# Kernel optimization log

Hardware: AMD Instinct MI355X
Metric: run time of the kernel (lower is better)

The kernel has to match this reference:

```python
import jax, jax.numpy as jnp
import numpy as np

ALPHA = 0.2  # LeakyReLU negative slope
MASK_VAL = -1e9


def setup_inputs() -> dict:
    key = jax.random.key(0)
    k1, k2, k3, k4 = jax.random.split(key, 4)
    B, N, F_in, F_out = 8, 2048, 512, 512
    h = jax.random.normal(k1, (B, N, F_in), dtype=jnp.float32)
    adj = jax.random.randint(k2, (B, N, N), 0, 2, dtype=jnp.int32)
    # xavier_uniform with gain=1.414
    def xavier(k, shape, gain=1.414):
        fan_in, fan_out = shape[0], shape[1]
        bound = gain * np.sqrt(6.0 / (fan_in + fan_out))
        return jax.random.uniform(k, shape, jnp.float32, -bound, bound)
    W = xavier(k3, (F_in, F_out))
    a = xavier(k4, (2 * F_out, 1))
    return {"h": h, "adj": adj, "W": W, "a": a}


def reference(h, adj, W, a):
    # h: [B,N,Fin], adj: [B,N,N], W: [Fin,Fout], a: [2*Fout,1]
    Fout = W.shape[1]
    Wh = jnp.matmul(h, W)  # [B,N,Fout]
    # Split 'a' into source/target halves: concat([Wh_i, Wh_j]) @ a
    #   == (Wh_i @ a1) + (Wh_j @ a2), avoiding the O(N^2*2F) concat tensor.
    a1 = a[:Fout, 0]   # [Fout]
    a2 = a[Fout:, 0]   # [Fout]
    e_i = jnp.einsum('bnf,f->bn', Wh, a1)  # [B,N] score contribution of node i
    e_j = jnp.einsum('bnf,f->bn', Wh, a2)  # [B,N] score contribution of node j
    e = e_i[:, :, None] + e_j[:, None, :]  # [B,N,N]
    e = jax.nn.leaky_relu(e, negative_slope=ALPHA)
    e = jnp.where(adj == 0, MASK_VAL, e)
    attention = jax.nn.softmax(e, axis=2)  # [B,N,N]
    h_prime = jnp.matmul(attention, Wh)    # [B,N,Fout]
    return jax.nn.elu(h_prime)
```

## Files before the change

### kernel.cpp

```cpp
#include <hip/hip_runtime.h>
#include <hip/hip_bf16.h>

#define ALPHA 0.2f
#define LOG2E 1.44269504088896340736f

typedef float  f32x4 __attribute__((ext_vector_type(4)));
typedef float  f32x2 __attribute__((ext_vector_type(2)));
typedef int    i32x4 __attribute__((ext_vector_type(4)));
typedef int    i32x2 __attribute__((ext_vector_type(2)));
typedef unsigned int u32x2 __attribute__((ext_vector_type(2)));

static __device__ __forceinline__ void mfma_bf16_16x16x32(f32x4& c, i32x4 a, i32x4 b) {
  asm("v_mfma_f32_16x16x32_bf16 %0, %1, %2, %0" : "+v"(c) : "v"(a), "v"(b));
}
static __device__ __forceinline__ unsigned short f2bf(float x) {
  __hip_bfloat16 b = __float2bfloat16(x);
  return *reinterpret_cast<unsigned short*>(&b);
}
static __device__ __forceinline__ unsigned int cvtpk(float lo, float hi) {
  unsigned int r;
  asm("v_cvt_pk_bf16_f32 %0, %1, %2" : "=v"(r) : "v"(lo), "v"(hi));
  return r;
}
static __device__ __forceinline__ float dot4(f32x4 a, f32x4 b) {
  return a.x*b.x + a.y*b.y + a.z*b.z + a.w*b.w;
}

__global__ __launch_bounds__(256) void k_setup(const float* __restrict__ W, const float* __restrict__ a,
                                               unsigned short* __restrict__ wt,
                                               float* __restrict__ v1, float* __restrict__ v2,
                                               float* __restrict__ eiej) {
  const int bid = blockIdx.x, tid = threadIdx.x;
  __shared__ float S[32][33];
  if (bid < 256) {
    const int k0 = (bid >> 4) * 32, f0 = (bid & 15) * 32;
    const int r = tid >> 5, c = tid & 31;
    #pragma unroll
    for (int rr = r; rr < 32; rr += 8) S[rr][c] = W[(size_t)(k0 + rr) * 512 + f0 + c];
    __syncthreads();
    #pragma unroll
    for (int rr = r; rr < 32; rr += 8) wt[(size_t)(f0 + rr) * 512 + k0 + c] = f2bf(S[c][rr]);
  } else if (bid < 384) {
    const int kk = (bid - 256) * 4 + (tid >> 6);
    const int l = tid & 63;
    const float* wr = W + (size_t)kk * 512 + l * 8;
    f32x4 w0 = *(const f32x4*)(wr),            w1 = *(const f32x4*)(wr + 4);
    f32x4 p0 = *(const f32x4*)(a + l*8),       p1 = *(const f32x4*)(a + l*8 + 4);
    f32x4 q0 = *(const f32x4*)(a + 512 + l*8), q1 = *(const f32x4*)(a + 512 + l*8 + 4);
    float s1 = dot4(w0,p0) + dot4(w1,p1);
    float s2 = dot4(w0,q0) + dot4(w1,q1);
    #pragma unroll
    for (int off = 1; off < 64; off <<= 1) { s1 += __shfl_xor(s1, off); s2 += __shfl_xor(s2, off); }
    if (l == 0) { v1[kk] = s1 * LOG2E; v2[kk] = s2 * LOG2E; }
  } else {
    const int idx = (bid - 384) * 1024 + tid * 4;
    *(f32x4*)(eiej + idx) = (f32x4){0.f,0.f,0.f,0.f};
  }
}

__global__ __launch_bounds__(256) void k_prep(const float* __restrict__ h,
                                              const float* __restrict__ v1, const float* __restrict__ v2,
                                              unsigned short* __restrict__ hT,
                                              float* __restrict__ ei, float* __restrict__ ej) {
  const int bid = blockIdx.x, tid = threadIdx.x;
  const int ft = bid & 15, nt = (bid >> 4) & 63, b = bid >> 10;
  __shared__ __align__(16) float S[32][36];

  const int n_loc = tid >> 3, fq = (tid & 7) * 4;
  const f32x4 v = __builtin_nontemporal_load(
      (const f32x4*)(h + (size_t)(b*2048 + nt*32 + n_loc)*512 + ft*32 + fq));
  *(f32x4*)&S[n_loc][fq] = v;

  const f32x4 a1 = *(const f32x4*)(v1 + ft*32 + fq);
  const f32x4 a2 = *(const f32x4*)(v2 + ft*32 + fq);
  float s1 = dot4(v, a1), s2 = dot4(v, a2);
  #pragma unroll
  for (int off = 1; off < 8; off <<= 1) { s1 += __shfl_xor(s1, off); s2 += __shfl_xor(s2, off); }
  if ((tid & 7) == 0) {
    atomicAdd(&ei[b*2048 + nt*32 + n_loc], s1);
    atomicAdd(&ej[b*2048 + nt*32 + n_loc], s2);
  }
  __syncthreads();

  const int f_loc = tid >> 3, nq = (tid & 7) * 4;
  u32x2 pk;
  pk.x = cvtpk(S[nq+0][f_loc], S[nq+1][f_loc]);
  pk.y = cvtpk(S[nq+2][f_loc], S[nq+3][f_loc]);
  *(u32x2*)(hT + (size_t)(b*512 + ft*32 + f_loc)*2048 + nt*32 + nq) = pk;
}

__global__ __launch_bounds__(512, 4) void k_attn(const int* __restrict__ adj,
                                                 const unsigned short* __restrict__ hT,
                                                 const float* __restrict__ ei, const float* __restrict__ ej,
                                                 unsigned short* __restrict__ C1) {
  const int tid = threadIdx.x;
  const int w = tid >> 6, l = tid & 63;
  const int fl = l & 15, kq = l >> 4;
  const int b = blockIdx.x & 7;
  const int i0 = (blockIdx.x >> 3) * 32;

  __shared__ __align__(16) unsigned short Plds[2][4096];
  __shared__ __align__(16) float ejl[2048];
  __shared__ __align__(16) float llds[32];

  *(f32x4*)&ejl[tid*4] = *(const f32x4*)(ej + b*2048 + tid*4);

  const int prow = w*4 + (l >> 4);
  const int pj   = (l & 15) * 8;
  const float eir = ei[b*2048 + i0 + prow];
  const int* aptr = adj + ((size_t)(b*2048 + i0 + prow) << 11) + pj;
  const int wboff = prow*256 + ((pj*2) ^ ((prow & 7) << 4));

  const unsigned short* bp[4];
  #pragma unroll
  for (int cf = 0; cf < 4; ++cf)
    bp[cf] = hT + (size_t)(b*512 + w*64 + cf*16 + fl) * 2048 + kq*8;
  const int zz = ((kq ^ (fl & 7)) << 4);
  const int arow0 = fl * 256, arow1 = (16 + fl) * 256;

  f32x4 acc[2][4];
  #pragma unroll
  for (int i = 0; i < 2; ++i)
    #pragma unroll
    for (int j = 0; j < 4; ++j) acc[i][j] = (f32x4){0.f,0.f,0.f,0.f};
  float sum = 0.f;

  i32x4 bcur[4];
  #pragma unroll
  for (int cf = 0; cf < 4; ++cf) bcur[cf] = *(const i32x4*)(bp[cf]);

  i32x4 pfa0 = __builtin_nontemporal_load((const i32x4*)(aptr));
  i32x4 pfa1 = __builtin_nontemporal_load((const i32x4*)(aptr + 4));
  i32x4 pfb0 = __builtin_nontemporal_load((const i32x4*)(aptr + 128));
  i32x4 pfb1 = __builtin_nontemporal_load((const i32x4*)(aptr + 128 + 4));

#define P_PHASE(BUFI, S, A0, A1) do {                                          \
    const f32x4 e0 = *(const f32x4*)&ejl[(S)*128 + pj];                        \
    const f32x4 e1 = *(const f32x4*)&ejl[(S)*128 + pj + 4];                    \
    float p[8];                                                                \
    _Pragma("unroll")                                                          \
    for (int e = 0; e < 8; ++e) {                                              \
      float x = eir + ((e < 4) ? e0[e] : e1[e-4]);                             \
      x = fmaxf(x, ALPHA * x);                                                 \
      const float pv = __builtin_amdgcn_exp2f(x);                              \
      const int av = (e < 4) ? (A0)[e] : (A1)[e-4];                            \
      p[e] = av ? pv : 0.f;                                                    \
      sum += p[e];                                                             \
    }                                                                          \
    i32x4 pk;                                                                  \
    pk.x = (int)cvtpk(p[0],p[1]); pk.y = (int)cvtpk(p[2],p[3]);                \
    pk.z = (int)cvtpk(p[4],p[5]); pk.w = (int)cvtpk(p[6],p[7]);                \
    *(i32x4*)((char*)&Plds[BUFI][0] + wboff) = pk;                             \
  } while (0)

#define MFMA_STEP(BUFI, S) do {                                                \
    const char* pb = (const char*)&Plds[BUFI][0];                              \
    _Pragma("unroll")                                                          \
    for (int kk = 0; kk < 4; ++kk) {                                           \
      const int t = (S)*4 + kk;                                                \
      const int tn = (t < 63) ? t + 1 : 63;                                    \
      i32x4 bnxt[4];                                                           \
      _Pragma("unroll")                                                        \
      for (int cf = 0; cf < 4; ++cf) bnxt[cf] = *(const i32x4*)(bp[cf] + tn*32); \
      const i32x4 af0 = *(const i32x4*)(pb + arow0 + ((kk << 6) ^ zz));        \
      const i32x4 af1 = *(const i32x4*)(pb + arow1 + ((kk << 6) ^ zz));        \
      _Pragma("unroll")                                                        \
      for (int cf = 0; cf < 4; ++cf) {                                         \
        mfma_bf16_16x16x32(acc[0][cf], af0, bcur[cf]);                         \
        mfma_bf16_16x16x32(acc[1][cf], af1, bcur[cf]);                         \
      }                                                                        \
      _Pragma("unroll")                                                        \
      for (int cf = 0; cf < 4; ++cf) bcur[cf] = bnxt[cf];                      \
    }                                                                          \
  } while (0)

  __syncthreads();
  P_PHASE(0, 0, pfa0, pfa1);
  pfa0 = __builtin_nontemporal_load((const i32x4*)(aptr + 2*128));
  pfa1 = __builtin_nontemporal_load((const i32x4*)(aptr + 2*128 + 4));
  __syncthreads();

  for (int ss = 0; ss < 8; ++ss) {
    const int s0 = ss*2, s1 = ss*2 + 1;
    MFMA_STEP(0, s0);
    P_PHASE(1, s0 + 1, pfb0, pfb1);
    if (s0 + 3 < 16) {
      pfb0 = __builtin_nontemporal_load((const i32x4*)(aptr + (s0+3)*128));
      pfb1 = __builtin_nontemporal_load((const i32x4*)(aptr + (s0+3)*128 + 4));
    }
    __syncthreads();
    MFMA_STEP(1, s1);
    if (s1 < 15) {
      P_PHASE(0, s1 + 1, pfa0, pfa1);
      if (s1 + 3 < 16) {
        pfa0 = __builtin_nontemporal_load((const i32x4*)(aptr + (s1+3)*128));
        pfa1 = __builtin_nontemporal_load((const i32x4*)(aptr + (s1+3)*128 + 4));
      }
    }
    __syncthreads();
  }
#undef P_PHASE
#undef MFMA_STEP

  sum += __shfl_xor(sum, 1);
  sum += __shfl_xor(sum, 2);
  sum += __shfl_xor(sum, 4);
  sum += __shfl_xor(sum, 8);
  if ((l & 15) == 0) llds[prow] = sum;
  __syncthreads();
  asm volatile("s_nop 7\ns_nop 7\ns_nop 7" :::);

  #pragma unroll
  for (int fr = 0; fr < 2; ++fr) {
    const f32x4 lv = *(const f32x4*)&llds[fr*16 + kq*4];
    f32x4 inv;
    inv.x = __builtin_amdgcn_rcpf(lv.x); inv.y = __builtin_amdgcn_rcpf(lv.y);
    inv.z = __builtin_amdgcn_rcpf(lv.z); inv.w = __builtin_amdgcn_rcpf(lv.w);
    #pragma unroll
    for (int cf = 0; cf < 4; ++cf) {
      const int f = w*64 + cf*16 + fl;
      unsigned short* cp = C1 + (size_t)(b*2048 + i0 + fr*16 + kq*4) * 512 + f;
      cp[0]    = f2bf(acc[fr][cf].x * inv.x);
      cp[512]  = f2bf(acc[fr][cf].y * inv.y);
      cp[1024] = f2bf(acc[fr][cf].z * inv.z);
      cp[1536] = f2bf(acc[fr][cf].w * inv.w);
    }
  }
}

__global__ __launch_bounds__(512, 2) void k_gemm2(const unsigned short* __restrict__ C1,
                                                  const unsigned short* __restrict__ wt,
                                                  float* __restrict__ out) {
  const int tid = threadIdx.x;
  const int w = tid >> 6, l = tid & 63;
  const int fl = l & 15, kq = l >> 4;
  const int row0 = (blockIdx.x & 7) * 2048 + (blockIdx.x >> 3) * 64;

  const unsigned short* ap[4];
  const unsigned short* bp[4];
  #pragma unroll
  for (int fr = 0; fr < 4; ++fr) ap[fr] = C1 + (size_t)(row0 + fr*16 + fl)*512 + kq*8;
  #pragma unroll
  for (int cf = 0; cf < 4; ++cf) bp[cf] = wt + (size_t)(w*64 + cf*16 + fl)*512 + kq*8;

  f32x4 acc[4][4];
  #pragma unroll
  for (int i = 0; i < 4; ++i)
    #pragma unroll
    for (int j = 0; j < 4; ++j) acc[i][j] = (f32x4){0.f,0.f,0.f,0.f};

  i32x4 ac[4], bc[4], an[4], bn[4];
  #pragma unroll
  for (int x = 0; x < 4; ++x) { ac[x] = *(const i32x4*)(ap[x]); bc[x] = *(const i32x4*)(bp[x]); }

  for (int sI = 0; sI < 16; ++sI) {
    const int sn = (sI < 15) ? sI + 1 : 15;
    #pragma unroll
    for (int x = 0; x < 4; ++x) {
      an[x] = *(const i32x4*)(ap[x] + sn*32);
      bn[x] = *(const i32x4*)(bp[x] + sn*32);
    }
    #pragma unroll
    for (int fr = 0; fr < 4; ++fr)
      #pragma unroll
      for (int cf = 0; cf < 4; ++cf)
        mfma_bf16_16x16x32(acc[fr][cf], ac[fr], bc[cf]);
    #pragma unroll
    for (int x = 0; x < 4; ++x) { ac[x] = an[x]; bc[x] = bn[x]; }
  }

  asm volatile("s_nop 7\ns_nop 7\ns_nop 7" :::);
  #pragma unroll
  for (int fr = 0; fr < 4; ++fr)
    #pragma unroll
    for (int cf = 0; cf < 4; ++cf) {
      const int f = w*64 + cf*16 + fl;
      float* op = out + (size_t)(row0 + fr*16 + kq*4) * 512 + f;
      const f32x4 v = acc[fr][cf];
      float o0 = v.x > 0.f ? v.x : __builtin_amdgcn_exp2f(v.x * LOG2E) - 1.f;
      float o1 = v.y > 0.f ? v.y : __builtin_amdgcn_exp2f(v.y * LOG2E) - 1.f;
      float o2 = v.z > 0.f ? v.z : __builtin_amdgcn_exp2f(v.z * LOG2E) - 1.f;
      float o3 = v.w > 0.f ? v.w : __builtin_amdgcn_exp2f(v.w * LOG2E) - 1.f;
      __builtin_nontemporal_store(o0, op);
      __builtin_nontemporal_store(o1, op + 512);
      __builtin_nontemporal_store(o2, op + 1024);
      __builtin_nontemporal_store(o3, op + 1536);
    }
}

extern "C" void kernel_launch(void* const* d_in, const int* in_sizes, int n_in,
                              void* d_out, int out_size, void* d_ws, size_t ws_size,
                              hipStream_t stream) {
  const float* h  = (const float*)d_in[0];
  const int*  adj = (const int*)d_in[1];
  const float* W  = (const float*)d_in[2];
  const float* a  = (const float*)d_in[3];
  float* out = (float*)d_out;
  char* ws = (char*)d_ws;
  unsigned short* wt = (unsigned short*)(ws);
  unsigned short* hT = (unsigned short*)(ws + 524288);
  unsigned short* C1 = (unsigned short*)(ws + 17301504);
  float* ei = (float*)(ws + 34078720);
  float* ej = (float*)(ws + 34144256);
  float* v1 = (float*)(ws + 34209792);
  float* v2 = (float*)(ws + 34211840);

  hipLaunchKernelGGL(k_setup, dim3(416),  dim3(256), 0, stream, W, a, wt, v1, v2, ei);
  hipLaunchKernelGGL(k_prep,  dim3(8192), dim3(256), 0, stream, h, v1, v2, hT, ei, ej);
  hipLaunchKernelGGL(k_attn,  dim3(512),  dim3(512), 0, stream, adj, hT, ei, ej, C1);
  hipLaunchKernelGGL(k_gemm2, dim3(256),  dim3(512), 0, stream, C1, wt, out);
}
```

Baseline: 362.7 us.

## Pack adjacency into bitmask and retile attention to 128-row, half-feature blocks

Result: faster. 324.9 us (-10.4%).

```diff
diff --git a/kernel.cpp b/kernel.cpp
--- a/kernel.cpp
+++ b/kernel.cpp
@@ -58,6 +58,25 @@
   }
 }
 
+__global__ __launch_bounds__(256) void k_pack(const int* __restrict__ adj,
+                                              unsigned short* __restrict__ adjb) {
+  const size_t g = (size_t)blockIdx.x * 256 + threadIdx.x;
+  const int* p = adj + g * 16;
+  const i32x4 v0 = __builtin_nontemporal_load((const i32x4*)(p));
+  const i32x4 v1 = __builtin_nontemporal_load((const i32x4*)(p + 4));
+  const i32x4 v2 = __builtin_nontemporal_load((const i32x4*)(p + 8));
+  const i32x4 v3 = __builtin_nontemporal_load((const i32x4*)(p + 12));
+  unsigned int m = 0;
+  #pragma unroll
+  for (int e = 0; e < 4; ++e) {
+    m |= ((unsigned)v0[e] & 1u) << e;
+    m |= ((unsigned)v1[e] & 1u) << (4 + e);
+    m |= ((unsigned)v2[e] & 1u) << (8 + e);
+    m |= ((unsigned)v3[e] & 1u) << (12 + e);
+  }
+  adjb[g] = (unsigned short)m;
+}
+
 __global__ __launch_bounds__(256) void k_prep(const float* __restrict__ h,
                                               const float* __restrict__ v1, const float* __restrict__ v2,
                                               unsigned short* __restrict__ hT,
@@ -89,68 +108,76 @@
   *(u32x2*)(hT + (size_t)(b*512 + ft*32 + f_loc)*2048 + nt*32 + nq) = pk;
 }
 
-__global__ __launch_bounds__(512, 4) void k_attn(const int* __restrict__ adj,
-                                                 const unsigned short* __restrict__ hT,
-                                                 const float* __restrict__ ei, const float* __restrict__ ej,
-                                                 unsigned short* __restrict__ C1) {
+__global__ __launch_bounds__(1024, 4) void k_attn(const unsigned short* __restrict__ adjb,
+                                                  const unsigned short* __restrict__ hT,
+                                                  const float* __restrict__ ei, const float* __restrict__ ej,
+                                                  unsigned short* __restrict__ C1) {
   const int tid = threadIdx.x;
   const int w = tid >> 6, l = tid & 63;
   const int fl = l & 15, kq = l >> 4;
-  const int b = blockIdx.x & 7;
-  const int i0 = (blockIdx.x >> 3) * 32;
-
-  __shared__ __align__(16) unsigned short Plds[2][4096];
+  const int bid = blockIdx.x;
+  const int fh = bid & 1;
+  const int b  = (bid >> 1) & 7;
+  const int i0 = (bid >> 4) * 128;
+
+  __shared__ __align__(16) unsigned short Plds[2][16384];
   __shared__ __align__(16) float ejl[2048];
-  __shared__ __align__(16) float llds[32];
-
-  *(f32x4*)&ejl[tid*4] = *(const f32x4*)(ej + b*2048 + tid*4);
-
-  const int prow = w*4 + (l >> 4);
-  const int pj   = (l & 15) * 8;
-  const float eir = ei[b*2048 + i0 + prow];
-  const int* aptr = adj + ((size_t)(b*2048 + i0 + prow) << 11) + pj;
-  const int wboff = prow*256 + ((pj*2) ^ ((prow & 7) << 4));
-
-  const unsigned short* bp[4];
-  #pragma unroll
-  for (int cf = 0; cf < 4; ++cf)
-    bp[cf] = hT + (size_t)(b*512 + w*64 + cf*16 + fl) * 2048 + kq*8;
-  const int zz = ((kq ^ (fl & 7)) << 4);
-  const int arow0 = fl * 256, arow1 = (16 + fl) * 256;
-
-  f32x4 acc[2][4];
-  #pragma unroll
-  for (int i = 0; i < 2; ++i)
-    #pragma unroll
-    for (int j = 0; j < 4; ++j) acc[i][j] = (f32x4){0.f,0.f,0.f,0.f};
+  __shared__ __align__(16) float llds[128];
+
+  if (tid < 512) *(f32x4*)&ejl[tid*4] = *(const f32x4*)(ej + b*2048 + tid*4);
+
+  const int pr = tid >> 3;
+  const int js = (tid & 7) * 16;
+  const float eir = ei[b*2048 + i0 + pr];
+  const char* abp = (const char*)adjb + (size_t)(b*2048 + i0 + pr) * 256 + (tid & 7) * 2;
+  const int swp = (pr & 7) << 4;
+  const int wb0 = pr*256 + ((js*2)      ^ swp);
+  const int wb1 = pr*256 + ((js*2 + 16) ^ swp);
+
+  const int mw = w >> 3, fw = w & 7;
+  const unsigned short* bp[2];
+  #pragma unroll
+  for (int cf = 0; cf < 2; ++cf)
+    bp[cf] = hT + (size_t)(b*512 + fh*256 + fw*32 + cf*16 + fl) * 2048 + kq*8;
+  const int swz = (fl & 7) << 4;
+  int abase[4];
+  #pragma unroll
+  for (int mf = 0; mf < 4; ++mf) abase[mf] = (mw*64 + mf*16 + fl) * 256;
+
+  f32x4 acc[4][2];
+  #pragma unroll
+  for (int i = 0; i < 4; ++i)
+    #pragma unroll
+    for (int j = 0; j < 2; ++j) acc[i][j] = (f32x4){0.f,0.f,0.f,0.f};
   float sum = 0.f;
 
-  i32x4 bcur[4];
-  #pragma unroll
-  for (int cf = 0; cf < 4; ++cf) bcur[cf] = *(const i32x4*)(bp[cf]);
-
-  i32x4 pfa0 = __builtin_nontemporal_load((const i32x4*)(aptr));
-  i32x4 pfa1 = __builtin_nontemporal_load((const i32x4*)(aptr + 4));
-  i32x4 pfb0 = __builtin_nontemporal_load((const i32x4*)(aptr + 128));
-  i32x4 pfb1 = __builtin_nontemporal_load((const i32x4*)(aptr + 128 + 4));
-
-#define P_PHASE(BUFI, S, A0, A1) do {                                          \
-    const f32x4 e0 = *(const f32x4*)&ejl[(S)*128 + pj];                        \
-    const f32x4 e1 = *(const f32x4*)&ejl[(S)*128 + pj + 4];                    \
-    float p[8];                                                                \
+  i32x4 bcur[2];
+  #pragma unroll
+  for (int cf = 0; cf < 2; ++cf) bcur[cf] = *(const i32x4*)(bp[cf]);
+
+#define P_PHASE(BUFI, S, BITS) do {                                            \
+    const f32x4 ev0 = *(const f32x4*)&ejl[(S)*128 + js];                       \
+    const f32x4 ev1 = *(const f32x4*)&ejl[(S)*128 + js + 4];                   \
+    const f32x4 ev2 = *(const f32x4*)&ejl[(S)*128 + js + 8];                   \
+    const f32x4 ev3 = *(const f32x4*)&ejl[(S)*128 + js + 12];                  \
+    float p[16];                                                               \
     _Pragma("unroll")                                                          \
-    for (int e = 0; e < 8; ++e) {                                              \
-      float x = eir + ((e < 4) ? e0[e] : e1[e-4]);                             \
-      x = fmaxf(x, ALPHA * x);                                                 \
+    for (int e = 0; e < 16; ++e) {                                             \
+      const float ejv = (e < 4) ? ev0[e] : (e < 8) ? ev1[e-4]                  \
+                       : (e < 12) ? ev2[e-8] : ev3[e-12];                      \
+      float x = eir + ejv;                                                     \
+      x = fmaxf(x, ALPHA * x);                       \
       const float pv = __builtin_amdgcn_exp2f(x);                              \
-      const int av = (e < 4) ? (A0)[e] : (A1)[e-4];                            \
-      p[e] = av ? pv : 0.f;                                                    \
+      p[e] = (((BITS) >> e) & 1u) ? pv : 0.f;                                  \
       sum += p[e];                                                             \
     }                                                                          \
-    i32x4 pk;                                                                  \
-    pk.x = (int)cvtpk(p[0],p[1]); pk.y = (int)cvtpk(p[2],p[3]);                \
-    pk.z = (int)cvtpk(p[4],p[5]); pk.w = (int)cvtpk(p[6],p[7]);                \
-    *(i32x4*)((char*)&Plds[BUFI][0] + wboff) = pk;                             \
+    i32x4 pk0, pk1;                                                            \
+    pk0.x = (int)cvtpk(p[0],p[1]);   pk0.y = (int)cvtpk(p[2],p[3]);            \
+    pk0.z = (int)cvtpk(p[4],p[5]);   pk0.w = (int)cvtpk(p[6],p[7]);            \
+    pk1.x = (int)cvtpk(p[8],p[9]);   pk1.y = (int)cvtpk(p[10],p[11]);          \
+    pk1.z = (int)cvtpk(p[12],p[13]); pk1.w = (int)cvtpk(p[14],p[15]);          \
+    *(i32x4*)((char*)&Plds[BUFI][0] + wb0) = pk0;                              \
+    *(i32x4*)((char*)&Plds[BUFI][0] + wb1) = pk1;                              \
   } while (0)
 
 #define MFMA_STEP(BUFI, S) do {                                                \
@@ -159,43 +186,37 @@
     for (int kk = 0; kk < 4; ++kk) {                                           \
       const int t = (S)*4 + kk;                                                \
       const int tn = (t < 63) ? t + 1 : 63;                                    \
-      i32x4 bnxt[4];                                                           \
+      i32x4 bnxt[2];                                                           \
       _Pragma("unroll")                                                        \
-      for (int cf = 0; cf < 4; ++cf) bnxt[cf] = *(const i32x4*)(bp[cf] + tn*32); \
-      const i32x4 af0 = *(const i32x4*)(pb + arow0 + ((kk << 6) ^ zz));        \
-      const i32x4 af1 = *(const i32x4*)(pb + arow1 + ((kk << 6) ^ zz));        \
+      for (int cf = 0; cf < 2; ++cf) bnxt[cf] = *(const i32x4*)(bp[cf] + tn*32); \
+      i32x4 af[4];                                                             \
       _Pragma("unroll")                                                        \
-      for (int cf = 0; cf < 4; ++cf) {                                         \
-        mfma_bf16_16x16x32(acc[0][cf], af0, bcur[cf]);                         \
-        mfma_bf16_16x16x32(acc[1][cf], af1, bcur[cf]);                         \
-      }                                                                        \
+      for (int mf = 0; mf < 4; ++mf)                                           \
+        af[mf] = *(const i32x4*)(pb + abase[mf] + ((kk*64 + kq*16) ^ swz));    \
       _Pragma("unroll")                                                        \
-      for (int cf = 0; cf < 4; ++cf) bcur[cf] = bnxt[cf];                      \
+      for (int mf = 0; mf < 4; ++mf)                                           \
+        _Pragma("unroll")                                                      \
+        for (int cf = 0; cf < 2; ++cf)                                         \
+          mfma_bf16_16x16x32(acc[mf][cf], af[mf], bcur[cf]);                   \
+      _Pragma("unroll")                                                        \
+      for (int cf = 0; cf < 2; ++cf) bcur[cf] = bnxt[cf];                      \
     }                                                                          \
   } while (0)
 
+  unsigned int bits = *(const unsigned short*)(abp);
   __syncthreads();
-  P_PHASE(0, 0, pfa0, pfa1);
-  pfa0 = __builtin_nontemporal_load((const i32x4*)(aptr + 2*128));
-  pfa1 = __builtin_nontemporal_load((const i32x4*)(aptr + 2*128 + 4));
+  P_PHASE(0, 0, bits);
+  bits = *(const unsigned short*)(abp + 16);
   __syncthreads();
 
-  for (int ss = 0; ss < 8; ++ss) {
-    const int s0 = ss*2, s1 = ss*2 + 1;
-    MFMA_STEP(0, s0);
-    P_PHASE(1, s0 + 1, pfb0, pfb1);
-    if (s0 + 3 < 16) {
-      pfb0 = __builtin_nontemporal_load((const i32x4*)(aptr + (s0+3)*128));
-      pfb1 = __builtin_nontemporal_load((const i32x4*)(aptr + (s0+3)*128 + 4));
-    }
-    __syncthreads();
-    MFMA_STEP(1, s1);
-    if (s1 < 15) {
-      P_PHASE(0, s1 + 1, pfa0, pfa1);
-      if (s1 + 3 < 16) {
-        pfa0 = __builtin_nontemporal_load((const i32x4*)(aptr + (s1+3)*128));
-        pfa1 = __builtin_nontemporal_load((const i32x4*)(aptr + (s1+3)*128 + 4));
-      }
+  for (int ssi = 0; ssi < 16; ++ssi) {
+    const int cur = ssi & 1;
+    MFMA_STEP(cur, ssi);
+    if (ssi < 15) {
+      const int sspf = (ssi + 2 < 16) ? ssi + 2 : 15;
+      const unsigned int bn = *(const unsigned short*)(abp + sspf*16);
+      P_PHASE(cur ^ 1, ssi + 1, bits);
+      bits = bn;
     }
     __syncthreads();
   }
@@ -205,25 +226,24 @@
   sum += __shfl_xor(sum, 1);
   sum += __shfl_xor(sum, 2);
   sum += __shfl_xor(sum, 4);
-  sum += __shfl_xor(sum, 8);
-  if ((l & 15) == 0) llds[prow] = sum;
+  if ((tid & 7) == 0) llds[pr] = sum;
   __syncthreads();
   asm volatile("s_nop 7\ns_nop 7\ns_nop 7" :::);
 
   #pragma unroll
-  for (int fr = 0; fr < 2; ++fr) {
-    const f32x4 lv = *(const f32x4*)&llds[fr*16 + kq*4];
+  for (int mf = 0; mf < 4; ++mf) {
+    const f32x4 lv = *(const f32x4*)&llds[mw*64 + mf*16 + kq*4];
     f32x4 inv;
     inv.x = __builtin_amdgcn_rcpf(lv.x); inv.y = __builtin_amdgcn_rcpf(lv.y);
     inv.z = __builtin_amdgcn_rcpf(lv.z); inv.w = __builtin_amdgcn_rcpf(lv.w);
     #pragma unroll
-    for (int cf = 0; cf < 4; ++cf) {
-      const int f = w*64 + cf*16 + fl;
-      unsigned short* cp = C1 + (size_t)(b*2048 + i0 + fr*16 + kq*4) * 512 + f;
-      cp[0]    = f2bf(acc[fr][cf].x * inv.x);
-      cp[512]  = f2bf(acc[fr][cf].y * inv.y);
-      cp[1024] = f2bf(acc[fr][cf].z * inv.z);
-      cp[1536] = f2bf(acc[fr][cf].w * inv.w);
+    for (int cf = 0; cf < 2; ++cf) {
+      const int f = fh*256 + fw*32 + cf*16 + fl;
+      unsigned short* cp = C1 + (size_t)(b*2048 + i0 + mw*64 + mf*16 + kq*4) * 512 + f;
+      cp[0]    = f2bf(acc[mf][cf].x * inv.x);
+      cp[512]  = f2bf(acc[mf][cf].y * inv.y);
+      cp[1024] = f2bf(acc[mf][cf].z * inv.z);
+      cp[1536] = f2bf(acc[mf][cf].w * inv.w);
     }
   }
 }
@@ -297,16 +317,18 @@
   const float* a  = (const float*)d_in[3];
   float* out = (float*)d_out;
   char* ws = (char*)d_ws;
-  unsigned short* wt = (unsigned short*)(ws);
-  unsigned short* hT = (unsigned short*)(ws + 524288);
-  unsigned short* C1 = (unsigned short*)(ws + 17301504);
-  float* ei = (float*)(ws + 34078720);
-  float* ej = (float*)(ws + 34144256);
-  float* v1 = (float*)(ws + 34209792);
-  float* v2 = (float*)(ws + 34211840);
-
-  hipLaunchKernelGGL(k_setup, dim3(416),  dim3(256), 0, stream, W, a, wt, v1, v2, ei);
-  hipLaunchKernelGGL(k_prep,  dim3(8192), dim3(256), 0, stream, h, v1, v2, hT, ei, ej);
-  hipLaunchKernelGGL(k_attn,  dim3(512),  dim3(512), 0, stream, adj, hT, ei, ej, C1);
-  hipLaunchKernelGGL(k_gemm2, dim3(256),  dim3(512), 0, stream, C1, wt, out);
-}
+  unsigned short* wt   = (unsigned short*)(ws);
+  unsigned short* hT   = (unsigned short*)(ws + 524288);
+  unsigned short* C1   = (unsigned short*)(ws + 17301504);
+  float* ei            = (float*)(ws + 34078720);
+  float* ej            = (float*)(ws + 34144256);
+  float* v1            = (float*)(ws + 34209792);
+  float* v2            = (float*)(ws + 34211840);
+  unsigned short* adjb = (unsigned short*)(ws + 34213888);
+
+  hipLaunchKernelGGL(k_setup, dim3(416),  dim3(256),  0, stream, W, a, wt, v1, v2, ei);
+  hipLaunchKernelGGL(k_pack,  dim3(8192), dim3(256),  0, stream, adj, adjb);
+  hipLaunchKernelGGL(k_prep,  dim3(8192), dim3(256),  0, stream, h, v1, v2, hT, ei, ej);
+  hipLaunchKernelGGL(k_attn,  dim3(256),  dim3(1024), 0, stream, adjb, hT, ei, ej, C1);
+  hipLaunchKernelGGL(k_gemm2, dim3(256),  dim3(512),  0, stream, C1, wt, out);
+}
```
